# Performance work log

Measured on AMD Instinct MI355X. Metric: run time of the kernel, lower is better.

Reference implementation:

```python
import jax, jax.numpy as jnp
import numpy as np

B, N, T, D, NEMB = 16, 64, 50, 4, 128  # batch, nodes, timesteps, in-dims, embed
EPS = 1e-20


def setup_inputs() -> dict:
    key = jax.random.key(0)
    ks = jax.random.split(key, 5)
    x = jax.random.normal(ks[0], (B, N, T, D), dtype=jnp.float32)
    # fully-connected directed graph without self loops: E = N*(N-1)
    send_idx, rec_idx = np.where(~np.eye(N, dtype=bool))
    eye = np.eye(N, dtype=np.float32)
    rel_send = jnp.asarray(eye[send_idx])  # [E, N] one-hot
    rel_rec = jnp.asarray(eye[rec_idx])    # [E, N] one-hot
    W_conv = jax.random.normal(ks[1], (D, NEMB), dtype=jnp.float32) / np.sqrt(D)
    b_conv = jax.random.normal(ks[2], (NEMB,), dtype=jnp.float32) * 0.01
    W_skip = jax.random.normal(ks[3], (D, NEMB), dtype=jnp.float32) / np.sqrt(D)
    b_skip = jax.random.normal(ks[4], (NEMB,), dtype=jnp.float32) * 0.01
    return dict(x=x, rel_rec=rel_rec, rel_send=rel_send,
                W_conv=W_conv, b_conv=b_conv, W_skip=W_skip, b_skip=b_skip)


def reference(x, rel_rec, rel_send, W_conv, b_conv, W_skip, b_skip):
    # gather endpoint features: [B, E, T, D]
    senders = jnp.einsum('en,bntd->betd', rel_send, x)
    receivers = jnp.einsum('en,bntd->betd', rel_rec, x)
    # per-edge inverse distance -> [B, T, E]
    spatial_norm = jnp.linalg.norm(receivers - senders, axis=-1)  # [B, E, T]
    adj_values = (1.0 / (spatial_norm + EPS)).transpose(0, 2, 1)   # [B, T, E]
    # rel_send.T @ diag(w) @ rel_rec, without the O(E^2) diag_embed: [B, T, N, N]
    adj = jnp.einsum('es,bte,er->btsr', rel_send, adj_values, rel_rec)
    # symmetric degree normalization D^{-1/2} A D^{-1/2} (no self loops)
    deg = adj.sum(-1)                      # [B, T, N]
    dinv = (deg + EPS) ** -0.5
    adj_n = dinv[..., :, None] * adj * dinv[..., None, :]
    # graph convolution branch
    xp = jnp.transpose(x, (0, 2, 1, 3))    # [B, T, N, D]
    x_conv = jnp.einsum('btnm,btmd->btnd', adj_n, xp) @ W_conv + b_conv
    x_conv = jnp.transpose(x_conv, (0, 2, 1, 3))  # [B, N, T, NEMB]
    # skip branch
    x_skip = x @ W_skip + b_skip           # [B, N, T, NEMB]
    return jax.nn.selu(jnp.concatenate([x_skip, x_conv], axis=-1))
```

## Files before the change

kernel.cpp:

```cpp
#include <hip/hip_runtime.h>
#include <hip/hip_bf16.h>

#define NB 16
#define NN 64
#define NT 50
#define ND 4
#define NE 128
#define CH 256

__device__ __forceinline__ float bf2f(unsigned short u) {
    union { unsigned int i; float f; } c;
    c.i = ((unsigned int)u) << 16;
    return c.f;
}

__device__ __forceinline__ unsigned short f2bf(float f) {
    union { float f; unsigned int i; } c;
    c.f = f;
    unsigned int x = c.i;
    x += 0x7fffu + ((x >> 16) & 1u);
    return (unsigned short)(x >> 16);
}

__device__ __forceinline__ float selu_f(float v) {
    const float scale = 1.0507009873554805f;
    const float alpha = 1.6732632423543772f;
    return v > 0.0f ? scale * v : scale * alpha * (__expf(v) - 1.0f);
}

__device__ __forceinline__ float4 ld4rt(bool isbf, const void* p, size_t off) {
    if (isbf) {
        const ushort4 v = *(const ushort4*)((const unsigned short*)p + off);
        return make_float4(bf2f(v.x), bf2f(v.y), bf2f(v.z), bf2f(v.w));
    }
    return *(const float4*)((const float*)p + off);
}

__device__ __forceinline__ void st4rt(bool isbf, void* p, size_t off, float4 r) {
    if (isbf) {
        *(ushort4*)((unsigned short*)p + off) =
            make_ushort4(f2bf(r.x), f2bf(r.y), f2bf(r.z), f2bf(r.w));
    } else {
        *(float4*)((float*)p + off) = r;
    }
}

__global__ __launch_bounds__(256) void gcn_kernel(
    const void* __restrict__ x, const void* __restrict__ rel,
    const void* __restrict__ Wc, const void* __restrict__ bc,
    const void* __restrict__ Ws, const void* __restrict__ bs,
    void* __restrict__ out)
{
    const bool isbf = (((const unsigned int*)rel)[0] != 0u);

    const int bt = blockIdx.x;
    const int b = bt / NT;
    const int t = bt - b * NT;
    const int tid = threadIdx.x;

    __shared__ float4 xt[NN];
    __shared__ float4 xsc[NN];
    __shared__ float part[256];
    __shared__ float dinv[NN];
    __shared__ float4 yp[NN][4];
    __shared__ float4 y4[NN];
    __shared__ float4 Wsm[ND * NE / 4];
    __shared__ float4 Wcm[ND * NE / 4];
    __shared__ float4 bsm[NE / 4];
    __shared__ float4 bcm[NE / 4];

    if (tid < 128) {
        Wsm[tid] = ld4rt(isbf, Ws, (size_t)tid * 4);
        Wcm[tid] = ld4rt(isbf, Wc, (size_t)tid * 4);
    } else if (tid < 160) {
        const int i = tid - 128;
        bsm[i] = ld4rt(isbf, bs, (size_t)i * 4);
        bcm[i] = ld4rt(isbf, bc, (size_t)i * 4);
    }
    if (tid < NN) {
        xt[tid] = ld4rt(isbf, x, (((size_t)b * NN + tid) * NT + t) * ND);
    }
    __syncthreads();

    const int n = tid >> 2;
    const int q = tid & 3;
    const float4 xn = xt[n];
    float av[16];
    float psum = 0.0f;
#pragma unroll
    for (int i = 0; i < 16; ++i) {
        const int m = (q << 4) + ((i + n) & 15);
        const float4 xm = xt[m];
        const float dx = xn.x - xm.x, dy = xn.y - xm.y;
        const float dz = xn.z - xm.z, dw = xn.w - xm.w;
        const float dist = sqrtf(dx * dx + dy * dy + dz * dz + dw * dw);
        const float v = (m == n) ? 0.0f : 1.0f / (dist + 1e-20f);
        av[i] = v;
        psum += v;
    }
    part[tid] = psum;
    __syncthreads();

    if (tid < NN) {
        const float deg = part[tid * 4] + part[tid * 4 + 1] +
                          part[tid * 4 + 2] + part[tid * 4 + 3];
        const float di = rsqrtf(deg + 1e-20f);
        dinv[tid] = di;
        const float4 v = xt[tid];
        xsc[tid] = make_float4(v.x * di, v.y * di, v.z * di, v.w * di);
    }
    __syncthreads();

    float4 acc = make_float4(0.f, 0.f, 0.f, 0.f);
#pragma unroll
    for (int i = 0; i < 16; ++i) {
        const int m = (q << 4) + ((i + n) & 15);
        const float w = av[i];
        const float4 xm = xsc[m];
        acc.x = fmaf(w, xm.x, acc.x);
        acc.y = fmaf(w, xm.y, acc.y);
        acc.z = fmaf(w, xm.z, acc.z);
        acc.w = fmaf(w, xm.w, acc.w);
    }
    yp[n][q] = acc;
    __syncthreads();

    if (tid < NN) {
        const float4 s0 = yp[tid][0], s1 = yp[tid][1];
        const float4 s2 = yp[tid][2], s3 = yp[tid][3];
        const float di = dinv[tid];
        y4[tid] = make_float4((s0.x + s1.x + s2.x + s3.x) * di,
                              (s0.y + s1.y + s2.y + s3.y) * di,
                              (s0.z + s1.z + s2.z + s3.z) * di,
                              (s0.w + s1.w + s2.w + s3.w) * di);
    }
    __syncthreads();

    const int j = tid & 63;
    const bool skipb = j < 32;
    const int jj = j & 31;
    const float4* wb = skipb ? Wsm : Wcm;
    const float4 w0 = wb[jj], w1 = wb[32 + jj], w2 = wb[64 + jj], w3 = wb[96 + jj];
    const float4 bias = skipb ? bsm[jj] : bcm[jj];
    const float4* inb = skipb ? xt : y4;
    const int nb0 = tid >> 6;

#pragma unroll
    for (int k = 0; k < 16; ++k) {
        const int nn = (k << 2) + nb0;
        const float4 in = inb[nn];
        float4 r = bias;
        r.x = fmaf(in.x, w0.x, fmaf(in.y, w1.x, fmaf(in.z, w2.x, fmaf(in.w, w3.x, r.x))));
        r.y = fmaf(in.x, w0.y, fmaf(in.y, w1.y, fmaf(in.z, w2.y, fmaf(in.w, w3.y, r.y))));
        r.z = fmaf(in.x, w0.z, fmaf(in.y, w1.z, fmaf(in.z, w2.z, fmaf(in.w, w3.z, r.z))));
        r.w = fmaf(in.x, w0.w, fmaf(in.y, w1.w, fmaf(in.z, w2.w, fmaf(in.w, w3.w, r.w))));
        r.x = selu_f(r.x);
        r.y = selu_f(r.y);
        r.z = selu_f(r.z);
        r.w = selu_f(r.w);
        st4rt(isbf, out, (((size_t)b * NN + nn) * NT + t) * CH + 4 * j, r);
    }
}

extern "C" void kernel_launch(void* const* d_in, const int* in_sizes, int n_in,
                              void* d_out, int out_size, void* d_ws, size_t ws_size,
                              hipStream_t stream) {
    const void* x   = d_in[0];
    const void* rel = d_in[1];
    const void* Wc  = d_in[3];
    const void* bc  = d_in[4];
    const void* Ws  = d_in[5];
    const void* bs  = d_in[6];
    gcn_kernel<<<dim3(NB * NT), dim3(256), 0, stream>>>(x, rel, Wc, bc, Ws, bs, d_out);
}
```

Measured before the change: 90.13 us.

## Use 512-thread blocks and wave shuffles for degree and aggregation reductions

Doubles the block to 512 threads, with 8 lanes per node instead of 4. The degree sum and the neighbour aggregation are now reduced with wave shuffles rather than shared-memory partial arrays. This removes two __syncthreads barriers and their shared buffers, and the node loads move to the last wave so they overlap with the weight loads. Each thread now writes 8 output rows instead of 16, which spreads the store-bound epilogue across more waves; the cost is fewer resident blocks per CU.

```diff
diff --git a/kernel.cpp b/kernel.cpp
--- a/kernel.cpp
+++ b/kernel.cpp
@@ -45,7 +45,7 @@
     }
 }
 
-__global__ __launch_bounds__(256) void gcn_kernel(
+__global__ __launch_bounds__(512) void gcn_kernel(
     const void* __restrict__ x, const void* __restrict__ rel,
     const void* __restrict__ Wc, const void* __restrict__ bc,
     const void* __restrict__ Ws, const void* __restrict__ bs,
@@ -60,9 +60,6 @@
 
     __shared__ float4 xt[NN];
     __shared__ float4 xsc[NN];
-    __shared__ float part[256];
-    __shared__ float dinv[NN];
-    __shared__ float4 yp[NN][4];
     __shared__ float4 y4[NN];
     __shared__ float4 Wsm[ND * NE / 4];
     __shared__ float4 Wcm[ND * NE / 4];
@@ -76,63 +73,58 @@
         const int i = tid - 128;
         bsm[i] = ld4rt(isbf, bs, (size_t)i * 4);
         bcm[i] = ld4rt(isbf, bc, (size_t)i * 4);
-    }
-    if (tid < NN) {
-        xt[tid] = ld4rt(isbf, x, (((size_t)b * NN + tid) * NT + t) * ND);
+    } else if (tid >= 448) {
+        const int nld = tid - 448;
+        xt[nld] = ld4rt(isbf, x, (((size_t)b * NN + nld) * NT + t) * ND);
     }
     __syncthreads();
 
-    const int n = tid >> 2;
-    const int q = tid & 3;
+    const int n = tid >> 3;
+    const int q = tid & 7;
     const float4 xn = xt[n];
-    float av[16];
+    float av[8];
     float psum = 0.0f;
 #pragma unroll
-    for (int i = 0; i < 16; ++i) {
-        const int m = (q << 4) + ((i + n) & 15);
+    for (int j = 0; j < 8; ++j) {
+        const int m = (j << 3) + ((q + j + n) & 7);
         const float4 xm = xt[m];
         const float dx = xn.x - xm.x, dy = xn.y - xm.y;
         const float dz = xn.z - xm.z, dw = xn.w - xm.w;
         const float dist = sqrtf(dx * dx + dy * dy + dz * dz + dw * dw);
         const float v = (m == n) ? 0.0f : 1.0f / (dist + 1e-20f);
-        av[i] = v;
+        av[j] = v;
         psum += v;
     }
-    part[tid] = psum;
-    __syncthreads();
+    psum += __shfl_xor(psum, 1);
+    psum += __shfl_xor(psum, 2);
+    psum += __shfl_xor(psum, 4);
+    const float di = rsqrtf(psum + 1e-20f);
 
-    if (tid < NN) {
-        const float deg = part[tid * 4] + part[tid * 4 + 1] +
-                          part[tid * 4 + 2] + part[tid * 4 + 3];
-        const float di = rsqrtf(deg + 1e-20f);
-        dinv[tid] = di;
-        const float4 v = xt[tid];
-        xsc[tid] = make_float4(v.x * di, v.y * di, v.z * di, v.w * di);
+    if (q == 0) {
+        xsc[n] = make_float4(xn.x * di, xn.y * di, xn.z * di, xn.w * di);
     }
     __syncthreads();
 
     float4 acc = make_float4(0.f, 0.f, 0.f, 0.f);
 #pragma unroll
-    for (int i = 0; i < 16; ++i) {
-        const int m = (q << 4) + ((i + n) & 15);
-        const float w = av[i];
+    for (int j = 0; j < 8; ++j) {
+        const int m = (j << 3) + ((q + j + n) & 7);
+        const float w = av[j];
         const float4 xm = xsc[m];
         acc.x = fmaf(w, xm.x, acc.x);
         acc.y = fmaf(w, xm.y, acc.y);
         acc.z = fmaf(w, xm.z, acc.z);
         acc.w = fmaf(w, xm.w, acc.w);
     }
-    yp[n][q] = acc;
-    __syncthreads();
-
-    if (tid < NN) {
-        const float4 s0 = yp[tid][0], s1 = yp[tid][1];
-        const float4 s2 = yp[tid][2], s3 = yp[tid][3];
-        const float di = dinv[tid];
-        y4[tid] = make_float4((s0.x + s1.x + s2.x + s3.x) * di,
-                              (s0.y + s1.y + s2.y + s3.y) * di,
-                              (s0.z + s1.z + s2.z + s3.z) * di,
-                              (s0.w + s1.w + s2.w + s3.w) * di);
+#pragma unroll
+    for (int s = 1; s <= 4; s <<= 1) {
+        acc.x += __shfl_xor(acc.x, s);
+        acc.y += __shfl_xor(acc.y, s);
+        acc.z += __shfl_xor(acc.z, s);
+        acc.w += __shfl_xor(acc.w, s);
+    }
+    if (q == 0) {
+        y4[n] = make_float4(acc.x * di, acc.y * di, acc.z * di, acc.w * di);
     }
     __syncthreads();
 
@@ -143,11 +135,11 @@
     const float4 w0 = wb[jj], w1 = wb[32 + jj], w2 = wb[64 + jj], w3 = wb[96 + jj];
     const float4 bias = skipb ? bsm[jj] : bcm[jj];
     const float4* inb = skipb ? xt : y4;
-    const int nb0 = tid >> 6;
+    const int w = tid >> 6;
 
 #pragma unroll
-    for (int k = 0; k < 16; ++k) {
-        const int nn = (k << 2) + nb0;
+    for (int rr = 0; rr < 8; ++rr) {
+        const int nn = (rr << 3) + w;
         const float4 in = inb[nn];
         float4 r = bias;
         r.x = fmaf(in.x, w0.x, fmaf(in.y, w1.x, fmaf(in.z, w2.x, fmaf(in.w, w3.x, r.x))));
@@ -171,5 +163,5 @@
     const void* bc  = d_in[4];
     const void* Ws  = d_in[5];
     const void* bs  = d_in[6];
-    gcn_kernel<<<dim3(NB * NT), dim3(256), 0, stream>>>(x, rel, Wc, bc, Ws, bs, d_out);
+    gcn_kernel<<<dim3(NB * NT), dim3(512), 0, stream>>>(x, rel, Wc, bc, Ws, bs, d_out);
 }
```

New measurement: 88.71 us. Within noise of the previous version (-1.6%).
